# Performance work log

Measured on AMD Instinct MI355X. Metric: run time of the kernel, lower is better.

## Reference

```python
import jax, jax.numpy as jnp
import numpy as np

D_THRESH = 0.5  # init arg `dist`


def setup_inputs() -> dict:
    key = jax.random.key(0)
    k1, k2 = jax.random.split(key)
    N, M, C = 20000, 25000, 3
    pointcloud = jax.random.uniform(k1, (N, C), dtype=jnp.float32)
    pointcloud_padding = jax.random.uniform(k2, (M, C), dtype=jnp.float32)
    return {"pointcloud": pointcloud, "pointcloud_padding": pointcloud_padding}


def reference(pointcloud, pointcloud_padding):
    # torch.cdist(padding, pointcloud): Euclidean distance matrix [M, N]
    # via the GEMM formulation ||a||^2 + ||b||^2 - 2 a.b (matches torch's path)
    a2 = jnp.sum(pointcloud_padding * pointcloud_padding, axis=1)[:, None]  # [M,1]
    b2 = jnp.sum(pointcloud * pointcloud, axis=1)[None, :]                  # [1,N]
    ab = pointcloud_padding @ pointcloud.T                                  # [M,N]
    dist = jnp.sqrt(jnp.maximum(a2 + b2 - 2.0 * ab, 0.0))                   # [M,N]
    # count neighbors within radius, per pointcloud point
    counts = jnp.sum(dist <= D_THRESH, axis=0).astype(jnp.int32)            # [N]
    out = counts.reshape(-1, 1)[: pointcloud.shape[0]]                      # [N,1]
    return out
```

## Files before the change

kernel.cpp:

```cpp
#include <hip/hip_runtime.h>

typedef short  bf16x8   __attribute__((ext_vector_type(8)));
typedef int    int32x4  __attribute__((ext_vector_type(4)));
typedef int    int32x16 __attribute__((ext_vector_type(16)));
typedef float  f32x16   __attribute__((ext_vector_type(16)));

#define JS      13
#define STREAMS (JS * 4)
#define TI      128
#define DEPTH   2

__device__ __forceinline__ unsigned short f2bf(float x) {
    unsigned u = __builtin_bit_cast(unsigned, x);
    u += 0x7FFF + ((u >> 16) & 1);
    return (unsigned short)(u >> 16);
}
__device__ __forceinline__ float bf2f(unsigned short h) {
    unsigned u = ((unsigned)h) << 16;
    return __builtin_bit_cast(float, u);
}

__global__ __launch_bounds__(256) void dens_pack_kernel(
    const float* __restrict__ pad, uint4* __restrict__ ws,
    int* __restrict__ out, int M, int mtot, int N)
{
    const int j = blockIdx.x * 256 + threadIdx.x;
    if (j < N) out[j] = 0;
    if (j >= mtot) return;

    float qx = 0.f, qy = 0.f, qz = 0.f;
    float negc = -1.0e6f;
    if (j < M) {
        qx = pad[3 * j]; qy = pad[3 * j + 1]; qz = pad[3 * j + 2];
        negc = 0.125f - 0.5f * (qx * qx + qy * qy + qz * qz);
    }
    const unsigned short xh = f2bf(qx), yh = f2bf(qy), zh = f2bf(qz);
    const unsigned short xl = f2bf(qx - bf2f(xh));
    const unsigned short yl = f2bf(qy - bf2f(yh));
    const unsigned short zl = f2bf(qz - bf2f(zh));
    const unsigned short ch = f2bf(negc);
    const unsigned short cl = f2bf(negc - bf2f(ch));

    uint4 p0, p1;
    p0.x = (unsigned)xh | ((unsigned)yh << 16);
    p0.y = (unsigned)zh | ((unsigned)xl << 16);
    p0.z = (unsigned)yl | ((unsigned)zl << 16);
    p0.w = (unsigned)xh | ((unsigned)yh << 16);
    p1.x = (unsigned)zh | ((unsigned)xl << 16);
    p1.y = (unsigned)yl | ((unsigned)zl << 16);
    p1.z = (unsigned)ch | ((unsigned)cl << 16);
    p1.w = 0x3F803F80u;
    ws[j]        = p0;
    ws[mtot + j] = p1;
}

__device__ __forceinline__ void make_bfrag(const float* __restrict__ pc,
                                           int i, int N, int half, bf16x8& B)
{
    float px = 0.f, py = 0.f, pz = 0.f;
    float ha = 3.0e38f;
    if (i < N) {
        px = pc[3 * i]; py = pc[3 * i + 1]; pz = pc[3 * i + 2];
        ha = 0.5f * (px * px + py * py + pz * pz);
    }
    const float nha = -ha;
    const unsigned short nhh = f2bf(nha);
    const unsigned short nhl = f2bf(nha - bf2f(nhh));
    const short xh = (short)f2bf(px), yh = (short)f2bf(py), zh = (short)f2bf(pz);
    const short xl = (short)f2bf(px - bf2f((unsigned short)xh));
    const short yl = (short)f2bf(py - bf2f((unsigned short)yh));
    const short zl = (short)f2bf(pz - bf2f((unsigned short)zh));
    const short ONE = (short)0x3F80;
    const bf16x8 Blo = {xh, yh, zh, xh, yh, zh, xl, yl};
    const bf16x8 Bhi = {zl, xl, yl, zl, ONE, ONE, (short)nhh, (short)nhl};
    B = half ? Bhi : Blo;
}

__device__ __forceinline__ unsigned pack4(float f0, float f1, float f2, float f3) {
    const unsigned u0 = __builtin_bit_cast(unsigned, f0);
    const unsigned u1 = __builtin_bit_cast(unsigned, f1);
    const unsigned u2 = __builtin_bit_cast(unsigned, f2);
    const unsigned u3 = __builtin_bit_cast(unsigned, f3);
    const unsigned lo = __builtin_amdgcn_perm(u0, u1, 0x0C0C0703u);
    const unsigned hi = __builtin_amdgcn_perm(u2, u3, 0x07030C0Cu);
    return (lo | hi) & 0x80808080u;
}

__device__ __forceinline__ int32x16 red_group(const f32x16 d, int32x4 m, int32x16 acc) {
    int32x4 P;
    P[0] = (int)pack4(d[0],  d[1],  d[2],  d[3]);
    P[1] = (int)pack4(d[4],  d[5],  d[6],  d[7]);
    P[2] = (int)pack4(d[8],  d[9],  d[10], d[11]);
    P[3] = (int)pack4(d[12], d[13], d[14], d[15]);
    return __builtin_amdgcn_mfma_i32_32x32x32_i8(P, m, acc, 0, 0, 0);
}

__global__ __launch_bounds__(256, 4) void dens_mfma_kernel(
    const float* __restrict__ pc,
    const char*  __restrict__ wsA,
    int* __restrict__ out,
    int N, int iters, int p1off, int visits)
{
    const int lane = threadIdx.x & 63;
    const int w    = threadIdx.x >> 6;
    const int n    = lane & 31;
    const int half = lane >> 5;

    const int ibase = blockIdx.x * TI;
    bf16x8 B0, B1, B2, B3;
    make_bfrag(pc, ibase + n,      N, half, B0);
    make_bfrag(pc, ibase + 32 + n, N, half, B1);
    make_bfrag(pc, ibase + 64 + n, N, half, B2);
    make_bfrag(pc, ibase + 96 + n, N, half, B3);

    const int gsel = n >> 3;
    const int m0 = (gsel == 0) ? 0x01010101 : 0;
    const int m1 = (gsel == 1) ? 0x01010101 : 0;
    const int m2 = (gsel == 2) ? 0x01010101 : 0;
    const int m3 = (gsel == 3) ? 0x01010101 : 0;
    const int32x4 R0 = {m0, m0, m0, m0};
    const int32x4 R1 = {m1, m1, m1, m1};
    const int32x4 R2 = {m2, m2, m2, m2};
    const int32x4 R3 = {m3, m3, m3, m3};

    const int stream = blockIdx.y * 4 + w;
    const uint4* __restrict__ ap = (const uint4*)
        (wsA + (half ? p1off : 0) + n * 16 + (size_t)stream * 512);
    const int T4 = 0x6800 / 16;

    const f32x16  z   = {0.f};
    int32x16      acc = {0};

    uint4 X = ap[0];
    uint4 Y = ap[T4];
    int nextoff = 2 * T4;

#define GROUPV(AV, BV, RV) { \
        f32x16 d = __builtin_amdgcn_mfma_f32_32x32x16_bf16(AV, BV, z, 0, 0, 0); \
        acc = red_group(d, RV, acc); }

    for (int t = 0; t < iters; ++t) {
        {
            const bf16x8 a = __builtin_bit_cast(bf16x8, X);
            GROUPV(a, B0, R0)
            GROUPV(a, B1, R1)
            GROUPV(a, B2, R2)
            GROUPV(a, B3, R3)
            X = ap[nextoff]; nextoff += T4;
        }
        {
            const bf16x8 a = __builtin_bit_cast(bf16x8, Y);
            GROUPV(a, B0, R0)
            GROUPV(a, B1, R1)
            GROUPV(a, B2, R2)
            GROUPV(a, B3, R3)
            Y = ap[nextoff]; nextoff += T4;
        }
    }
#undef GROUPV

    const int base = 32 * visits;
    __shared__ int red[4][TI];
    if ((lane & 7) == 0) {
        const int g   = n >> 3;
        const int hi4 = half << 2;
        int* rw = &red[w][32 * g];
        rw[ 0 + hi4] = base + (acc[0]  >> 7);
        rw[ 1 + hi4] = base + (acc[1]  >> 7);
        rw[ 2 + hi4] = base + (acc[2]  >> 7);
        rw[ 3 + hi4] = base + (acc[3]  >> 7);
        rw[ 8 + hi4] = base + (acc[4]  >> 7);
        rw[ 9 + hi4] = base + (acc[5]  >> 7);
        rw[10 + hi4] = base + (acc[6]  >> 7);
        rw[11 + hi4] = base + (acc[7]  >> 7);
        rw[16 + hi4] = base + (acc[8]  >> 7);
        rw[17 + hi4] = base + (acc[9]  >> 7);
        rw[18 + hi4] = base + (acc[10] >> 7);
        rw[19 + hi4] = base + (acc[11] >> 7);
        rw[24 + hi4] = base + (acc[12] >> 7);
        rw[25 + hi4] = base + (acc[13] >> 7);
        rw[26 + hi4] = base + (acc[14] >> 7);
        rw[27 + hi4] = base + (acc[15] >> 7);
    }
    __syncthreads();
    if (threadIdx.x < TI) {
        const int ii = ibase + threadIdx.x;
        if (ii < N) {
            const int s = red[0][threadIdx.x] + red[1][threadIdx.x] +
                          red[2][threadIdx.x] + red[3][threadIdx.x];
            atomicAdd(&out[ii], s);
        }
    }
}

extern "C" void kernel_launch(void* const* d_in, const int* in_sizes, int n_in,
                              void* d_out, int out_size, void* d_ws, size_t ws_size,
                              hipStream_t stream) {
    const float* pc  = (const float*)d_in[0];
    const float* pad = (const float*)d_in[1];
    int* out = (int*)d_out;

    const int N = in_sizes[0] / 3;
    const int M = in_sizes[1] / 3;
    const int jt = (M + 31) / 32;
    int visits = (jt + STREAMS - 1) / STREAMS;
    if (visits & 1) visits++;
    const int jtp  = (visits + DEPTH) * STREAMS;
    const int mtot = jtp * 32;

    dens_pack_kernel<<<(mtot + 255) / 256, 256, 0, stream>>>(
        pad, (uint4*)d_ws, out, M, mtot, N);

    dim3 grid((N + TI - 1) / TI, JS);
    dens_mfma_kernel<<<grid, 256, 0, stream>>>(
        pc, (const char*)d_ws, out, N, visits / 2, mtot * 16, visits);
}
```

Measured before the change: 82.27 us.

## Double per-block point tile to 256 to reuse each loaded A fragment more

Each wave now holds eight B fragments, covering 256 pointcloud points instead of 128, and issues eight MFMA groups per loaded padding fragment into two integer accumulators. The aim is to halve the global A-fragment loads per unit of compute and raise MFMA density per load. The costs are more registers (launch bounds lowered to 3 waves per SIMD), half as many blocks in the x dimension (about 79 for N=20000, times 13), and a longer dependency chain per iteration.

```diff
diff --git a/kernel.cpp b/kernel.cpp
--- a/kernel.cpp
+++ b/kernel.cpp
@@ -7,7 +7,7 @@
 
 #define JS      13
 #define STREAMS (JS * 4)
-#define TI      128
+#define TI      256
 #define DEPTH   2
 
 __device__ __forceinline__ unsigned short f2bf(float x) {
@@ -95,7 +95,7 @@
     return __builtin_amdgcn_mfma_i32_32x32x32_i8(P, m, acc, 0, 0, 0);
 }
 
-__global__ __launch_bounds__(256, 4) void dens_mfma_kernel(
+__global__ __launch_bounds__(256, 3) void dens_mfma_kernel(
     const float* __restrict__ pc,
     const char*  __restrict__ wsA,
     int* __restrict__ out,
@@ -107,11 +107,15 @@
     const int half = lane >> 5;
 
     const int ibase = blockIdx.x * TI;
-    bf16x8 B0, B1, B2, B3;
-    make_bfrag(pc, ibase + n,      N, half, B0);
-    make_bfrag(pc, ibase + 32 + n, N, half, B1);
-    make_bfrag(pc, ibase + 64 + n, N, half, B2);
-    make_bfrag(pc, ibase + 96 + n, N, half, B3);
+    bf16x8 B0, B1, B2, B3, B4, B5, B6, B7;
+    make_bfrag(pc, ibase + n,       N, half, B0);
+    make_bfrag(pc, ibase + 32 + n,  N, half, B1);
+    make_bfrag(pc, ibase + 64 + n,  N, half, B2);
+    make_bfrag(pc, ibase + 96 + n,  N, half, B3);
+    make_bfrag(pc, ibase + 128 + n, N, half, B4);
+    make_bfrag(pc, ibase + 160 + n, N, half, B5);
+    make_bfrag(pc, ibase + 192 + n, N, half, B6);
+    make_bfrag(pc, ibase + 224 + n, N, half, B7);
 
     const int gsel = n >> 3;
     const int m0 = (gsel == 0) ? 0x01010101 : 0;
@@ -128,32 +132,41 @@
         (wsA + (half ? p1off : 0) + n * 16 + (size_t)stream * 512);
     const int T4 = 0x6800 / 16;
 
-    const f32x16  z   = {0.f};
-    int32x16      acc = {0};
+    const f32x16  z    = {0.f};
+    int32x16      acc  = {0};
+    int32x16      acc2 = {0};
 
     uint4 X = ap[0];
     uint4 Y = ap[T4];
     int nextoff = 2 * T4;
 
-#define GROUPV(AV, BV, RV) { \
+#define GROUPV(AV, BV, RV, AC) { \
         f32x16 d = __builtin_amdgcn_mfma_f32_32x32x16_bf16(AV, BV, z, 0, 0, 0); \
-        acc = red_group(d, RV, acc); }
+        AC = red_group(d, RV, AC); }
 
     for (int t = 0; t < iters; ++t) {
         {
             const bf16x8 a = __builtin_bit_cast(bf16x8, X);
-            GROUPV(a, B0, R0)
-            GROUPV(a, B1, R1)
-            GROUPV(a, B2, R2)
-            GROUPV(a, B3, R3)
+            GROUPV(a, B0, R0, acc)
+            GROUPV(a, B1, R1, acc)
+            GROUPV(a, B2, R2, acc)
+            GROUPV(a, B3, R3, acc)
+            GROUPV(a, B4, R0, acc2)
+            GROUPV(a, B5, R1, acc2)
+            GROUPV(a, B6, R2, acc2)
+            GROUPV(a, B7, R3, acc2)
             X = ap[nextoff]; nextoff += T4;
         }
         {
             const bf16x8 a = __builtin_bit_cast(bf16x8, Y);
-            GROUPV(a, B0, R0)
-            GROUPV(a, B1, R1)
-            GROUPV(a, B2, R2)
-            GROUPV(a, B3, R3)
+            GROUPV(a, B0, R0, acc)
+            GROUPV(a, B1, R1, acc)
+            GROUPV(a, B2, R2, acc)
+            GROUPV(a, B3, R3, acc)
+            GROUPV(a, B4, R0, acc2)
+            GROUPV(a, B5, R1, acc2)
+            GROUPV(a, B6, R2, acc2)
+            GROUPV(a, B7, R3, acc2)
             Y = ap[nextoff]; nextoff += T4;
         }
     }
@@ -164,26 +177,43 @@
     if ((lane & 7) == 0) {
         const int g   = n >> 3;
         const int hi4 = half << 2;
-        int* rw = &red[w][32 * g];
-        rw[ 0 + hi4] = base + (acc[0]  >> 7);
-        rw[ 1 + hi4] = base + (acc[1]  >> 7);
-        rw[ 2 + hi4] = base + (acc[2]  >> 7);
-        rw[ 3 + hi4] = base + (acc[3]  >> 7);
-        rw[ 8 + hi4] = base + (acc[4]  >> 7);
-        rw[ 9 + hi4] = base + (acc[5]  >> 7);
-        rw[10 + hi4] = base + (acc[6]  >> 7);
-        rw[11 + hi4] = base + (acc[7]  >> 7);
-        rw[16 + hi4] = base + (acc[8]  >> 7);
-        rw[17 + hi4] = base + (acc[9]  >> 7);
-        rw[18 + hi4] = base + (acc[10] >> 7);
-        rw[19 + hi4] = base + (acc[11] >> 7);
-        rw[24 + hi4] = base + (acc[12] >> 7);
-        rw[25 + hi4] = base + (acc[13] >> 7);
-        rw[26 + hi4] = base + (acc[14] >> 7);
-        rw[27 + hi4] = base + (acc[15] >> 7);
+        int* rw  = &red[w][32 * g];
+        int* rw2 = &red[w][128 + 32 * g];
+        rw [ 0 + hi4] = base + (acc[0]   >> 7);
+        rw [ 1 + hi4] = base + (acc[1]   >> 7);
+        rw [ 2 + hi4] = base + (acc[2]   >> 7);
+        rw [ 3 + hi4] = base + (acc[3]   >> 7);
+        rw [ 8 + hi4] = base + (acc[4]   >> 7);
+        rw [ 9 + hi4] = base + (acc[5]   >> 7);
+        rw [10 + hi4] = base + (acc[6]   >> 7);
+        rw [11 + hi4] = base + (acc[7]   >> 7);
+        rw [16 + hi4] = base + (acc[8]   >> 7);
+        rw [17 + hi4] = base + (acc[9]   >> 7);
+        rw [18 + hi4] = base + (acc[10]  >> 7);
+        rw [19 + hi4] = base + (acc[11]  >> 7);
+        rw [24 + hi4] = base + (acc[12]  >> 7);
+        rw [25 + hi4] = base + (acc[13]  >> 7);
+        rw [26 + hi4] = base + (acc[14]  >> 7);
+        rw [27 + hi4] = base + (acc[15]  >> 7);
+        rw2[ 0 + hi4] = base + (acc2[0]  >> 7);
+        rw2[ 1 + hi4] = base + (acc2[1]  >> 7);
+        rw2[ 2 + hi4] = base + (acc2[2]  >> 7);
+        rw2[ 3 + hi4] = base + (acc2[3]  >> 7);
+        rw2[ 8 + hi4] = base + (acc2[4]  >> 7);
+        rw2[ 9 + hi4] = base + (acc2[5]  >> 7);
+        rw2[10 + hi4] = base + (acc2[6]  >> 7);
+        rw2[11 + hi4] = base + (acc2[7]  >> 7);
+        rw2[16 + hi4] = base + (acc2[8]  >> 7);
+        rw2[17 + hi4] = base + (acc2[9]  >> 7);
+        rw2[18 + hi4] = base + (acc2[10] >> 7);
+        rw2[19 + hi4] = base + (acc2[11] >> 7);
+        rw2[24 + hi4] = base + (acc2[12] >> 7);
+        rw2[25 + hi4] = base + (acc2[13] >> 7);
+        rw2[26 + hi4] = base + (acc2[14] >> 7);
+        rw2[27 + hi4] = base + (acc2[15] >> 7);
     }
     __syncthreads();
-    if (threadIdx.x < TI) {
+    {
         const int ii = ibase + threadIdx.x;
         if (ii < N) {
             const int s = red[0][threadIdx.x] + red[1][threadIdx.x] +
```

Measured after the change: 87.58 us. 1.06x slower.
